# Optimization experiments

Measured on AMD Instinct MI355X. Metric: run time of the kernel, lower is better.

Reference implementation:

```python
import jax, jax.numpy as jnp
from jax import lax
import numpy as np

N_LAYERS = 4
D_MODEL = 512
EXPAND = 3
D_INNER = EXPAND * D_MODEL  # 1536
D_STATE = 32
D_CONV = 4
DT_RANK = (D_MODEL + 15) // 16  # 32 (mamba default ceil(d_model/16))
BATCH = 1024
N_FEAT = 68
N_RAIN = 4
N_NONRAIN = N_FEAT - N_RAIN  # 64


def setup_inputs() -> dict:
    key = jax.random.key(0)
    ks = iter(jax.random.split(key, 40))

    def w(shape, s=0.02):
        return jax.random.normal(next(ks), shape, dtype=jnp.float32) * s

    inp = {
        'x': jax.random.normal(next(ks), (BATCH, N_FEAT), dtype=jnp.float32),
        # mamba_input_proj: Linear(64 -> d_model)
        'w_in': w((D_MODEL, N_NONRAIN)), 'b_in': jnp.zeros((D_MODEL,), jnp.float32),
        # per-layer LayerNorms
        'ln_g': jnp.ones((N_LAYERS, D_MODEL), jnp.float32),
        'ln_b': jnp.zeros((N_LAYERS, D_MODEL), jnp.float32),
        # Mamba per-layer params (stacked over layers)
        'W_inproj': w((N_LAYERS, 2 * D_INNER, D_MODEL)),
        'conv_w': w((N_LAYERS, D_INNER, D_CONV), 0.1),
        'conv_b': jnp.zeros((N_LAYERS, D_INNER), jnp.float32),
        'W_xproj': w((N_LAYERS, DT_RANK + 2 * D_STATE, D_INNER)),
        'W_dt': w((N_LAYERS, D_INNER, DT_RANK), 0.1),
        'b_dt': w((N_LAYERS, D_INNER), 0.5),
        'A_log': jnp.broadcast_to(jnp.log(jnp.arange(1, D_STATE + 1, dtype=jnp.float32)), (N_LAYERS, D_INNER, D_STATE)) + 0.0,
        'D_skip': jnp.ones((N_LAYERS, D_INNER), jnp.float32),
        'W_outproj': w((N_LAYERS, D_MODEL, D_INNER)),
        # logistic branch: Linear(4 -> 1) + sigmoid
        'w_log': w((1, N_RAIN), 0.1), 'b_log': jnp.zeros((1,), jnp.float32),
        # gate_proj: Linear(1 -> d_model)
        'W_gate': w((D_MODEL, 1), 0.1), 'b_gate': jnp.zeros((D_MODEL,), jnp.float32),
        # output head: Linear(d_model->32), ReLU, Linear(32->1)
        'W_h1': w((32, D_MODEL)), 'b_h1': jnp.zeros((32,), jnp.float32),
        'W_h2': w((1, 32)), 'b_h2': jnp.zeros((1,), jnp.float32),
    }
    return inp


def _layernorm(x, g, b, eps=1e-5):
    mu = x.mean(-1, keepdims=True)
    var = x.var(-1, keepdims=True)
    return (x - mu) * lax.rsqrt(var + eps) * g + b


def _mamba(x, Win, cw, cb, Wx, Wdt, bdt, Alog, Dp, Wout):
    # x: [B, L, d_model]
    B_, L, _ = x.shape
    xz = jnp.einsum('bld,ed->ble', x, Win)           # [B,L,2*d_inner]
    xc, z = jnp.split(xz, 2, axis=-1)
    # causal depthwise conv1d over L
    xt = jnp.pad(xc.transpose(0, 2, 1), ((0, 0), (0, 0), (D_CONV - 1, 0)))
    conv = lax.conv_general_dilated(xt, cw[:, None, :], (1,), 'VALID',
                                    dimension_numbers=('NCH', 'OIH', 'NCH'),
                                    feature_group_count=D_INNER)
    u = jax.nn.silu((conv + cb[None, :, None]).transpose(0, 2, 1))  # [B,L,d_inner]
    x_dbl = jnp.einsum('bld,ed->ble', u, Wx)         # [B,L,dt_rank+2*d_state]
    dt = x_dbl[..., :DT_RANK]
    Bm = x_dbl[..., DT_RANK:DT_RANK + D_STATE]
    Cm = x_dbl[..., DT_RANK + D_STATE:]
    delta = jax.nn.softplus(jnp.einsum('blr,dr->bld', dt, Wdt) + bdt)  # [B,L,d_inner]
    A = -jnp.exp(Alog)                               # [d_inner, d_state]
    dA = jnp.exp(jnp.einsum('bld,dn->bldn', delta, A))
    dBu = jnp.einsum('bld,bln->bldn', delta * u, Bm)

    def step(h, inp):
        dA_t, dBu_t, C_t = inp
        h = dA_t * h + dBu_t                         # [B,d_inner,d_state]
        return h, jnp.einsum('bdn,bn->bd', h, C_t)

    h0 = jnp.zeros((B_, D_INNER, D_STATE), x.dtype)
    _, ys = lax.scan(step, h0, (dA.transpose(1, 0, 2, 3), dBu.transpose(1, 0, 2, 3), Cm.transpose(1, 0, 2)))
    y = ys.transpose(1, 0, 2) + u * Dp               # [B,L,d_inner]
    y = y * jax.nn.silu(z)
    return jnp.einsum('bld,ed->ble', y, Wout)        # [B,L,d_model]


def reference(x, w_in, b_in, ln_g, ln_b, W_inproj, conv_w, conv_b, W_xproj, W_dt, b_dt,
              A_log, D_skip, W_outproj, w_log, b_log, W_gate, b_gate, W_h1, b_h1, W_h2, b_h2):
    rain = x[:, :N_RAIN]
    nonrain = x[:, N_RAIN:]
    h = jax.nn.relu(nonrain @ w_in.T + b_in)[:, None, :]   # [B,1,d_model]
    for l in range(N_LAYERS):
        res = h
        hn = _layernorm(h, ln_g[l], ln_b[l])
        hn = _mamba(hn, W_inproj[l], conv_w[l], conv_b[l], W_xproj[l], W_dt[l], b_dt[l],
                    A_log[l], D_skip[l], W_outproj[l])
        h = res + hn  # dropout is identity in eval mode
    m = h[:, 0, :]
    lg = jax.nn.sigmoid(rain @ w_log.T + b_log)            # [B,1]
    gate = lg @ W_gate.T + b_gate                          # [B,d_model]
    fused = m * gate
    z1 = jax.nn.relu(fused @ W_h1.T + b_h1)
    logits = (z1 @ W_h2.T + b_h2)[:, 0]
    return jax.nn.sigmoid(logits)
```

## Files before the change

### kernel.cpp

```cpp
#include <hip/hip_runtime.h>

typedef unsigned short u16;
typedef short v8s __attribute__((ext_vector_type(8)));
typedef float v4f __attribute__((ext_vector_type(4)));
typedef u16  v4u __attribute__((ext_vector_type(4)));

__device__ __forceinline__ float bf2f(u16 h){ return __uint_as_float(((unsigned)h)<<16); }
__device__ __forceinline__ u16 f2bf(float f){
  unsigned u = __float_as_uint(f);
  u += 0x7FFFu + ((u>>16)&1u);
  return (u16)(u>>16);
}
__device__ __forceinline__ float siluf(float x){ return x/(1.f+__expf(-x)); }
__device__ __forceinline__ float softplusf(float x){
  return (x>15.f) ? x : __logf(1.f+__expf(x));
}

struct SetupP {
  const float *x,*w_in,*b_in,*ln_g,*ln_b,*W_inproj,*W_xproj,*W_dt,*W_outproj;
  u16 *wIn,*wX,*wDt,*wOut;
  float *sg,*cb,*h;
  u16 *hb;
};

__global__ __launch_bounds__(256) void setup_kernel(SetupP sp)
{
  __shared__ u16 As[64*72], Bs[64*72];
  const int blk = blockIdx.x, t = threadIdx.x;
  if(blk < 9984){
    const int c0=6291456, c1=c0+589824, c2=c1+196608;
    int i4 = (blk*256 + t)*4;
    float4 v; u16* dst;
    if(i4 < c0){
      v = *(const float4*)(sp.W_inproj + i4);
      int k = i4 & 511, l = (i4>>9)/3072;
      const float* gg = sp.ln_g + l*512 + k;
      v.x*=gg[0]; v.y*=gg[1]; v.z*=gg[2]; v.w*=gg[3];
      dst = sp.wIn + i4;
    } else if(i4 < c1){ int o=i4-c0; v=*(const float4*)(sp.W_xproj+o);   dst=sp.wX+o; }
    else if(i4 < c2){   int o=i4-c1; v=*(const float4*)(sp.W_dt+o);      dst=sp.wDt+o; }
    else {              int o=i4-c2; v=*(const float4*)(sp.W_outproj+o); dst=sp.wOut+o; }
    v4u pk={ f2bf(v.x), f2bf(v.y), f2bf(v.z), f2bf(v.w) };
    *(v4u*)dst = pk;
    return;
  }
  if(blk < 13056){
    int wid=t>>6, lane=t&63;
    int ridx = (blk-9984)*4 + wid;
    int l = ridx/3072;
    const float* wr = sp.W_inproj + (size_t)ridx*512;
    const float* gg = sp.ln_g + l*512;
    const float* bb = sp.ln_b + l*512;
    float sgv=0.f, cbv=0.f;
#pragma unroll
    for(int i=0;i<8;i++){ int k=lane*8+i; float w=wr[k]; sgv+=gg[k]*w; cbv+=bb[k]*w; }
#pragma unroll
    for(int off=1; off<64; off<<=1){ sgv+=__shfl_xor(sgv,off); cbv+=__shfl_xor(cbv,off); }
    if(lane==0){ sp.sg[ridx]=sgv; sp.cb[ridx]=cbv; }
    return;
  }
  const int mb=blk-13056, mt=mb>>3, nt=mb&7;
  const int m0=mt*64, n0=nt*64;
  const int lane=t&63, wid=t>>6;
  const int wm=wid>>1, wn=wid&1, qd=lane>>4, lr=lane&15;
  const int r=t>>2, cq=t&3;
  {
    const float4* ax=(const float4*)(sp.x + (size_t)(m0+r)*68 + 4 + cq*16);
    const float4* bx=(const float4*)(sp.w_in + (size_t)(n0+r)*64 + cq*16);
    float4 av0=ax[0], av1=ax[1], av2=ax[2], av3=ax[3];
    float4 bv0=bx[0], bv1=bx[1], bv2=bx[2], bv3=bx[3];
    v4u pa0={f2bf(av0.x),f2bf(av0.y),f2bf(av0.z),f2bf(av0.w)};
    v4u pa1={f2bf(av1.x),f2bf(av1.y),f2bf(av1.z),f2bf(av1.w)};
    v4u pa2={f2bf(av2.x),f2bf(av2.y),f2bf(av2.z),f2bf(av2.w)};
    v4u pa3={f2bf(av3.x),f2bf(av3.y),f2bf(av3.z),f2bf(av3.w)};
    v4u pb0={f2bf(bv0.x),f2bf(bv0.y),f2bf(bv0.z),f2bf(bv0.w)};
    v4u pb1={f2bf(bv1.x),f2bf(bv1.y),f2bf(bv1.z),f2bf(bv1.w)};
    v4u pb2={f2bf(bv2.x),f2bf(bv2.y),f2bf(bv2.z),f2bf(bv2.w)};
    v4u pb3={f2bf(bv3.x),f2bf(bv3.y),f2bf(bv3.z),f2bf(bv3.w)};
    u16* aw=As+r*72+cq*16; u16* bw=Bs+r*72+cq*16;
    *(v4u*)(aw)=pa0; *(v4u*)(aw+4)=pa1; *(v4u*)(aw+8)=pa2; *(v4u*)(aw+12)=pa3;
    *(v4u*)(bw)=pb0; *(v4u*)(bw+4)=pb1; *(v4u*)(bw+8)=pb2; *(v4u*)(bw+12)=pb3;
  }
  __syncthreads();
  v4f acc[2][2];
#pragma unroll
  for(int i=0;i<2;i++)
#pragma unroll
    for(int j=0;j<2;j++) acc[i][j]=v4f{0.f,0.f,0.f,0.f};
#pragma unroll
  for(int s=0;s<2;s++){
    v8s af[2], bfv[2];
#pragma unroll
    for(int i=0;i<2;i++) af[i] =*(const v8s*)(As+(wm*32+i*16+lr)*72+s*32+qd*8);
#pragma unroll
    for(int j=0;j<2;j++) bfv[j]=*(const v8s*)(Bs+(wn*32+j*16+lr)*72+s*32+qd*8);
#pragma unroll
    for(int i=0;i<2;i++)
#pragma unroll
      for(int j=0;j<2;j++)
        acc[i][j]=__builtin_amdgcn_mfma_f32_16x16x32_bf16(af[i],bfv[j],acc[i][j],0,0,0);
  }
#pragma unroll
  for(int i=0;i<2;i++)
#pragma unroll
    for(int j=0;j<2;j++){
      const int gb0=m0+wm*32+i*16+qd*4;
      const int ge =n0+wn*32+j*16+lr;
#pragma unroll
      for(int rr=0;rr<4;rr++){
        float hv=fmaxf(acc[i][j][rr]+sp.b_in[ge],0.f);
        const size_t idx=(size_t)(gb0+rr)*512+ge;
        sp.h[idx]=hv; sp.hb[idx]=f2bf(hv);
      }
    }
}

__global__ __launch_bounds__(256) void gemm1_ln(
  const u16* __restrict__ hb, const u16* __restrict__ Wp,
  const float* __restrict__ sg, const float* __restrict__ cb,
  const float* __restrict__ convw, const float* __restrict__ convb,
  u16* __restrict__ u, u16* __restrict__ zs)
{
  __shared__ u16 As[64*72], Bs[64*72];
  __shared__ float sS1[64], sS2[64];
  const int tid=threadIdx.x, lane=tid&63, wid=tid>>6;
  const int wm=wid>>1, wn=wid&1, qd=lane>>4, lr=lane&15;
  const int m0=blockIdx.y*64, n0=blockIdx.x*64;
  const int r_=tid>>2, cq=tid&3;
  const u16* Ap = hb + (size_t)(m0+r_)*512 + cq*16;
  const u16* Bp = Wp + (size_t)(n0+r_)*512 + cq*16;
  u16* Asw = As + r_*72 + cq*16;
  u16* Bsw = Bs + r_*72 + cq*16;

  v4f acc[2][2];
#pragma unroll
  for(int i=0;i<2;i++)
#pragma unroll
    for(int j=0;j<2;j++) acc[i][j]=v4f{0.f,0.f,0.f,0.f};
  float s1=0.f, s2=0.f;

  auto statAcc=[&](v8s v){
#pragma unroll
    for(int e=0;e<8;e++){ float f=bf2f((u16)v[e]); s1+=f; s2+=f*f; }
  };
  auto domfma=[&](){
#pragma unroll
    for(int s=0;s<2;s++){
      v8s af[2], bfv[2];
#pragma unroll
      for(int i=0;i<2;i++) af[i] =*(const v8s*)(As+(wm*32+i*16+lr)*72+s*32+qd*8);
#pragma unroll
      for(int j=0;j<2;j++) bfv[j]=*(const v8s*)(Bs+(wn*32+j*16+lr)*72+s*32+qd*8);
#pragma unroll
      for(int i=0;i<2;i++)
#pragma unroll
        for(int j=0;j<2;j++)
          acc[i][j]=__builtin_amdgcn_mfma_f32_16x16x32_bf16(af[i],bfv[j],acc[i][j],0,0,0);
    }
  };

  v8s a0a=*(const v8s*)(Ap),    a0b=*(const v8s*)(Ap+8);
  v8s b0a=*(const v8s*)(Bp),    b0b=*(const v8s*)(Bp+8);
  v8s a1a=*(const v8s*)(Ap+64), a1b=*(const v8s*)(Ap+72);
  v8s b1a=*(const v8s*)(Bp+64), b1b=*(const v8s*)(Bp+72);
  for(int c=0;c<8;c+=2){
    __syncthreads();
    *(v8s*)Asw=a0a; *(v8s*)(Asw+8)=a0b;
    *(v8s*)Bsw=b0a; *(v8s*)(Bsw+8)=b0b;
    statAcc(a0a); statAcc(a0b);
    __syncthreads();
    if(c+2<8){
      a0a=*(const v8s*)(Ap+(c+2)*64); a0b=*(const v8s*)(Ap+(c+2)*64+8);
      b0a=*(const v8s*)(Bp+(c+2)*64); b0b=*(const v8s*)(Bp+(c+2)*64+8);
    }
    domfma();
    __syncthreads();
    *(v8s*)Asw=a1a; *(v8s*)(Asw+8)=a1b;
    *(v8s*)Bsw=b1a; *(v8s*)(Bsw+8)=b1b;
    statAcc(a1a); statAcc(a1b);
    __syncthreads();
    if(c+3<8){
      a1a=*(const v8s*)(Ap+(c+3)*64); a1b=*(const v8s*)(Ap+(c+3)*64+8);
      b1a=*(const v8s*)(Bp+(c+3)*64); b1b=*(const v8s*)(Bp+(c+3)*64+8);
    }
    domfma();
  }

  s1+=__shfl_xor(s1,1); s2+=__shfl_xor(s2,1);
  s1+=__shfl_xor(s1,2); s2+=__shfl_xor(s2,2);
  if(cq==0){ sS1[r_]=s1; sS2[r_]=s2; }
  __syncthreads();

#pragma unroll
  for(int i=0;i<2;i++){
    const int lb0=wm*32+i*16+qd*4;
#pragma unroll
    for(int r=0;r<4;r++){
      const int lb=lb0+r, gb=m0+lb;
      float mu=sS1[lb]*(1.f/512.f);
      float rs=rsqrtf(sS2[lb]*(1.f/512.f)-mu*mu+1e-5f);
#pragma unroll
      for(int j=0;j<2;j++){
        const int ge=n0+wn*32+j*16+lr;
        float val = rs*(acc[i][j][r] - mu*sg[ge]) + cb[ge];
        if(ge<1536){
          u[(size_t)gb*1536+ge]=f2bf(siluf(val*convw[ge*4+3]+convb[ge]));
        }else{
          zs[(size_t)gb*1536+(ge-1536)]=f2bf(siluf(val));
        }
      }
    }
  }
}

__global__ __launch_bounds__(256) void gemm2(
  const u16* __restrict__ A, const u16* __restrict__ wX,
  float* __restrict__ xpart)
{
  __shared__ u16 As[64*40];
  __shared__ u16 Bs[96*40];
  const int tid=threadIdx.x, lane=tid&63, wid=tid>>6;
  const int wm=wid>>1, wn=wid&1, qd=lane>>4, lr=lane&15;
  const int m0=blockIdx.y*64;
  const int k0=blockIdx.x*192;
  const int r_=tid>>2, kg_=tid&3;
  const u16* Ap  = A  + (size_t)(m0+r_)*1536 + k0 + kg_*8;
  const u16* Bp0 = wX + (size_t)r_*1536      + k0 + kg_*8;
  const u16* Bp1 = wX + (size_t)(64+r_)*1536 + k0 + kg_*8;
  u16* Asw  = As + r_*40 + kg_*8;
  u16* Bsw0 = Bs + r_*40 + kg_*8;
  u16* Bsw1 = Bs + (64+r_)*40 + kg_*8;
  const bool hasB1 = tid<128;

  v4f acc[2][3];
#pragma unroll
  for(int i=0;i<2;i++)
#pragma unroll
    for(int j=0;j<3;j++) acc[i][j]=v4f{0.f,0.f,0.f,0.f};

  auto domfma=[&](){
    v8s af[2], bfv[3];
#pragma unroll
    for(int i=0;i<2;i++) af[i] =*(const v8s*)(As+(wm*32+i*16+lr)*40+qd*8);
#pragma unroll
    for(int j=0;j<3;j++) bfv[j]=*(const v8s*)(Bs+(wn*48+j*16+lr)*40+qd*8);
#pragma unroll
    for(int i=0;i<2;i++)
#pragma unroll
      for(int j=0;j<3;j++)
        acc[i][j]=__builtin_amdgcn_mfma_f32_16x16x32_bf16(af[i],bfv[j],acc[i][j],0,0,0);
  };

  v8s a0=*(const v8s*)(Ap),    b0x=*(const v8s*)(Bp0),    b0y{};
  v8s a1=*(const v8s*)(Ap+32), b1x=*(const v8s*)(Bp0+32), b1y{};
  if(hasB1){ b0y=*(const v8s*)(Bp1); b1y=*(const v8s*)(Bp1+32); }
  for(int it=0; it<6; it+=2){
    const int kk=it*32;
    __syncthreads();
    *(v8s*)Asw=a0; *(v8s*)Bsw0=b0x; if(hasB1) *(v8s*)Bsw1=b0y;
    __syncthreads();
    if(it+2<6){ a0=*(const v8s*)(Ap+kk+64); b0x=*(const v8s*)(Bp0+kk+64);
      if(hasB1) b0y=*(const v8s*)(Bp1+kk+64); }
    domfma();
    __syncthreads();
    *(v8s*)Asw=a1; *(v8s*)Bsw0=b1x; if(hasB1) *(v8s*)Bsw1=b1y;
    __syncthreads();
    if(it+2<6){ a1=*(const v8s*)(Ap+kk+96); b1x=*(const v8s*)(Bp0+kk+96);
      if(hasB1) b1y=*(const v8s*)(Bp1+kk+96); }
    domfma();
  }

  float* op = xpart + (size_t)blockIdx.x*98304;
#pragma unroll
  for(int i=0;i<2;i++)
#pragma unroll
    for(int j=0;j<3;j++){
      const int gb0=m0+wm*32+i*16+qd*4;
      const int ge =wn*48+j*16+lr;
#pragma unroll
      for(int r=0;r<4;r++)
        op[(size_t)(gb0+r)*96+ge]=acc[i][j][r];
    }
}

__global__ __launch_bounds__(256) void gemm3(
  const float* __restrict__ xpart, const u16* __restrict__ wDt,
  const float* __restrict__ bdt, const float* __restrict__ Dp,
  const u16* __restrict__ u, const u16* __restrict__ zs,
  u16* __restrict__ y)
{
  __shared__ u16 dts[64*40];
  __shared__ u16 Bs[64*40];
  __shared__ float sbl[64];
  const int tid=threadIdx.x, lane=tid&63, wid=tid>>6;
  const int wm=wid>>1, wn=wid&1, qd=lane>>4, lr=lane&15;
  const int m0=blockIdx.y*64, n0=blockIdx.x*64;
  const int r=tid>>2, sub=tid&3;

  v8s breg = *(const v8s*)(wDt + (size_t)(n0+r)*32 + sub*8);

  float a24[24];
#pragma unroll
  for(int i=0;i<24;i++) a24[i]=0.f;
#pragma unroll
  for(int z=0;z<8;z++){
    const float4* bz=(const float4*)(xpart + (size_t)z*98304 + (size_t)(m0+r)*96);
#pragma unroll
    for(int t=0;t<6;t++){
      float4 v=bz[sub+4*t];
      a24[4*t]+=v.x; a24[4*t+1]+=v.y; a24[4*t+2]+=v.z; a24[4*t+3]+=v.w;
    }
  }
  float s_=0.f;
#pragma unroll
  for(int m=0;m<4;m++) s_ += a24[8+m]*a24[16+m] + a24[12+m]*a24[20+m];
  s_ += __shfl_xor(s_,1); s_ += __shfl_xor(s_,2);
  if(sub==0) sbl[r]=s_;
  v4u p0={ f2bf(a24[0]), f2bf(a24[1]), f2bf(a24[2]), f2bf(a24[3]) };
  v4u p1={ f2bf(a24[4]), f2bf(a24[5]), f2bf(a24[6]), f2bf(a24[7]) };
  *(v4u*)(dts + r*40 + 4*sub)      = p0;
  *(v4u*)(dts + r*40 + 16 + 4*sub) = p1;
  *(v8s*)(Bs + r*40 + sub*8) = breg;
  __syncthreads();

  v4f acc[2][2];
#pragma unroll
  for(int i=0;i<2;i++)
#pragma unroll
    for(int j=0;j<2;j++) acc[i][j]=v4f{0.f,0.f,0.f,0.f};
  v8s af[2], bfv[2];
#pragma unroll
  for(int i=0;i<2;i++) af[i] =*(const v8s*)(dts+(wm*32+i*16+lr)*40+qd*8);
#pragma unroll
  for(int j=0;j<2;j++) bfv[j]=*(const v8s*)(Bs+(wn*32+j*16+lr)*40+qd*8);
#pragma unroll
  for(int i=0;i<2;i++)
#pragma unroll
    for(int j=0;j<2;j++)
      acc[i][j]=__builtin_amdgcn_mfma_f32_16x16x32_bf16(af[i],bfv[j],acc[i][j],0,0,0);

#pragma unroll
  for(int i=0;i<2;i++){
    const int lb0=wm*32+i*16+qd*4;
#pragma unroll
    for(int rr=0;rr<4;rr++){
      const int gb=m0+lb0+rr;
      const float sv=sbl[lb0+rr];
#pragma unroll
      for(int j=0;j<2;j++){
        const int ge=n0+wn*32+j*16+lr;
        float delta=softplusf(acc[i][j][rr]+bdt[ge]);
        float uu=bf2f(u[(size_t)gb*1536+ge]);
        float zz=bf2f(zs[(size_t)gb*1536+ge]);
        y[(size_t)gb*1536+ge]=f2bf(uu*(delta*sv+Dp[ge])*zz);
      }
    }
  }
}

__global__ __launch_bounds__(256) void gemm4(
  const u16* __restrict__ yv, const u16* __restrict__ wO,
  float* __restrict__ h, u16* __restrict__ hb)
{
  __shared__ u16 As[32*72], Bs[32*72];
  const int tid=threadIdx.x, lane=tid&63, wid=tid>>6;
  const int wm=wid>>1, wn=wid&1, qd=lane>>4, lr=lane&15;
  const int m0=blockIdx.y*32, n0=blockIdx.x*32;
  const int half=tid>>7, ts=tid&127;
  const int r_=ts>>2, cq=ts&3;
  const u16* Gp = (half ? wO + (size_t)(n0+r_)*1536
                        : yv + (size_t)(m0+r_)*1536) + cq*16;
  u16* Sw = (half ? Bs : As) + r_*72 + cq*16;

  v4f acc=v4f{0.f,0.f,0.f,0.f};
  auto domfma=[&](){
#pragma unroll
    for(int s=0;s<2;s++){
      v8s af=*(const v8s*)(As+(wm*16+lr)*72+s*32+qd*8);
      v8s bf=*(const v8s*)(Bs+(wn*16+lr)*72+s*32+qd*8);
      acc=__builtin_amdgcn_mfma_f32_16x16x32_bf16(af,bf,acc,0,0,0);
    }
  };

  v8s g0a=*(const v8s*)(Gp),    g0b=*(const v8s*)(Gp+8);
  v8s g1a=*(const v8s*)(Gp+64), g1b=*(const v8s*)(Gp+72);
  for(int c=0;c<24;c+=2){
    __syncthreads();
    *(v8s*)Sw=g0a; *(v8s*)(Sw+8)=g0b;
    __syncthreads();
    if(c+2<24){ g0a=*(const v8s*)(Gp+(c+2)*64); g0b=*(const v8s*)(Gp+(c+2)*64+8); }
    domfma();
    __syncthreads();
    *(v8s*)Sw=g1a; *(v8s*)(Sw+8)=g1b;
    __syncthreads();
    if(c+3<24){ g1a=*(const v8s*)(Gp+(c+3)*64); g1b=*(const v8s*)(Gp+(c+3)*64+8); }
    domfma();
  }

#pragma unroll
  for(int r=0;r<4;r++){
    const int gb=m0+wm*16+qd*4+r;
    const int ge=n0+wn*16+lr;
    const size_t idx=(size_t)gb*512+ge;
    float hv=h[idx]+acc[r];
    h[idx]=hv; hb[idx]=f2bf(hv);
  }
}

__global__ __launch_bounds__(256) void head_kernel(
  const float* __restrict__ x, const float* __restrict__ h,
  const float* __restrict__ wlog, const float* __restrict__ blog,
  const float* __restrict__ wg, const float* __restrict__ bg,
  const float* __restrict__ wh1, const float* __restrict__ bh1,
  const float* __restrict__ wh2, const float* __restrict__ bh2,
  float* __restrict__ out)
{
  int b = blockIdx.x, t = threadIdx.x;
  __shared__ float fused[512];
  __shared__ float part[256];
  __shared__ float z1s[32];
  float lgin = x[b*68+0]*wlog[0] + x[b*68+1]*wlog[1]
             + x[b*68+2]*wlog[2] + x[b*68+3]*wlog[3] + blog[0];
  float lg = 1.f/(1.f+__expf(-lgin));
  for(int d=t; d<512; d+=256)
    fused[d] = h[(size_t)b*512+d]*(lg*wg[d] + bg[d]);
  __syncthreads();
  int j = t&31, c = t>>5;
  float p = 0.f;
#pragma unroll
  for(int i=0;i<64;i++){ int d = c*64+i; p += fused[d]*wh1[j*512+d]; }
  part[t] = p;
  __syncthreads();
  if(t < 32){
    float z = bh1[t];
#pragma unroll
    for(int cc=0; cc<8; cc++) z += part[cc*32+t];
    z1s[t] = fmaxf(z, 0.f);
  }
  __syncthreads();
  if(t==0){
    float lo = bh2[0];
#pragma unroll
    for(int jj=0;jj<32;jj++) lo += z1s[jj]*wh2[jj];
    out[b] = 1.f/(1.f+__expf(-lo));
  }
}

extern "C" void kernel_launch(void* const* d_in, const int* in_sizes, int n_in,
                              void* d_out, int out_size, void* d_ws, size_t ws_size,
                              hipStream_t stream)
{
  const float* x        = (const float*)d_in[0];
  const float* w_in     = (const float*)d_in[1];
  const float* b_in     = (const float*)d_in[2];
  const float* ln_g     = (const float*)d_in[3];
  const float* ln_b     = (const float*)d_in[4];
  const float* W_inproj = (const float*)d_in[5];
  const float* conv_w   = (const float*)d_in[6];
  const float* conv_b   = (const float*)d_in[7];
  const float* W_xproj  = (const float*)d_in[8];
  const float* W_dt     = (const float*)d_in[9];
  const float* b_dt     = (const float*)d_in[10];
  const float* D_skip   = (const float*)d_in[12];
  const float* W_outproj= (const float*)d_in[13];
  const float* w_log    = (const float*)d_in[14];
  const float* b_log    = (const float*)d_in[15];
  const float* W_gate   = (const float*)d_in[16];
  const float* b_gate   = (const float*)d_in[17];
  const float* W_h1     = (const float*)d_in[18];
  const float* b_h1     = (const float*)d_in[19];
  const float* W_h2     = (const float*)d_in[20];
  const float* b_h2     = (const float*)d_in[21];
  float* out = (float*)d_out;
  (void)in_sizes; (void)n_in; (void)out_size; (void)ws_size;

  char* ws = (char*)d_ws;
  size_t off = 0;
  auto alloc = [&](size_t bytes)->char*{
    char* p = ws + off; off = (off + bytes + 255) & ~(size_t)255; return p; };
  u16*   wIn  = (u16*)  alloc(6291456u*2);
  u16*   wX   = (u16*)  alloc(589824u*2);
  u16*   wDt  = (u16*)  alloc(196608u*2);
  u16*   wOut = (u16*)  alloc(3145728u*2);
  float* sg   = (float*)alloc(12288u*4);
  float* cb   = (float*)alloc(12288u*4);
  float* h    = (float*)alloc(524288u*4);
  u16*   hb   = (u16*)  alloc(524288u*2);
  u16*   u    = (u16*)  alloc(1572864u*2);
  u16*   zs   = (u16*)  alloc(1572864u*2);
  u16*   y    = (u16*)  alloc(1572864u*2);
  float* xpart= (float*)alloc(8u*98304u*4);

  SetupP sp;
  sp.x=x; sp.w_in=w_in; sp.b_in=b_in; sp.ln_g=ln_g; sp.ln_b=ln_b;
  sp.W_inproj=W_inproj; sp.W_xproj=W_xproj; sp.W_dt=W_dt; sp.W_outproj=W_outproj;
  sp.wIn=wIn; sp.wX=wX; sp.wDt=wDt; sp.wOut=wOut;
  sp.sg=sg; sp.cb=cb; sp.h=h; sp.hb=hb;

  setup_kernel<<<13184,256,0,stream>>>(sp);

  for(int l=0;l<4;l++){
    gemm1_ln<<<dim3(48,16),256,0,stream>>>(
      hb, wIn+(size_t)l*1572864, sg+l*3072, cb+l*3072,
      conv_w+l*6144, conv_b+l*1536, u, zs);
    gemm2<<<dim3(8,16),256,0,stream>>>(
      u, wX+(size_t)l*147456, xpart);
    gemm3<<<dim3(24,16),256,0,stream>>>(
      xpart, wDt+(size_t)l*49152, b_dt+l*1536, D_skip+l*1536, u, zs, y);
    gemm4<<<dim3(16,32),256,0,stream>>>(
      y, wOut+(size_t)l*786432, h, hb);
  }

  head_kernel<<<1024,256,0,stream>>>(x, h, w_log, b_log, W_gate, b_gate,
                                     W_h1, b_h1, W_h2, b_h2, out);
}
```

Before: 288.4 us.

## Enlarge gemm1 M tile to 128 rows and double gemm4 K step

The input-projection GEMM with fused LayerNorm now covers 128 batch rows per block instead of 64, so each wave computes a 64x32 output from more accumulators and each weight tile loaded is reused across twice as many rows. The grid is halved in the y dimension to match. The output-projection GEMM now stages a K chunk of 128 per iteration instead of 64, which halves the number of barrier pairs and widens each load. In exchange, registers and shared memory per block go up and there are fewer blocks, which may reduce occupancy and leave some compute units idle.

```diff
diff --git a/kernel.cpp b/kernel.cpp
--- a/kernel.cpp
+++ b/kernel.cpp
@@ -121,20 +121,21 @@
   const float* __restrict__ convw, const float* __restrict__ convb,
   u16* __restrict__ u, u16* __restrict__ zs)
 {
-  __shared__ u16 As[64*72], Bs[64*72];
-  __shared__ float sS1[64], sS2[64];
+  __shared__ u16 As[128*72], Bs[64*72];
+  __shared__ float sS1[128], sS2[128];
   const int tid=threadIdx.x, lane=tid&63, wid=tid>>6;
   const int wm=wid>>1, wn=wid&1, qd=lane>>4, lr=lane&15;
-  const int m0=blockIdx.y*64, n0=blockIdx.x*64;
-  const int r_=tid>>2, cq=tid&3;
-  const u16* Ap = hb + (size_t)(m0+r_)*512 + cq*16;
-  const u16* Bp = Wp + (size_t)(n0+r_)*512 + cq*16;
-  u16* Asw = As + r_*72 + cq*16;
-  u16* Bsw = Bs + r_*72 + cq*16;
-
-  v4f acc[2][2];
-#pragma unroll
-  for(int i=0;i<2;i++)
+  const int m0=blockIdx.y*128, n0=blockIdx.x*64;
+  const int rA=tid>>1, cqA=tid&1;
+  const u16* Ap = hb + (size_t)(m0+rA)*512 + cqA*32;
+  u16* Asw = As + rA*72 + cqA*32;
+  const int rB=tid>>2, cqB=tid&3;
+  const u16* Bp = Wp + (size_t)(n0+rB)*512 + cqB*16;
+  u16* Bsw = Bs + rB*72 + cqB*16;
+
+  v4f acc[4][2];
+#pragma unroll
+  for(int i=0;i<4;i++)
 #pragma unroll
     for(int j=0;j<2;j++) acc[i][j]=v4f{0.f,0.f,0.f,0.f};
   float s1=0.f, s2=0.f;
@@ -146,54 +147,65 @@
   auto domfma=[&](){
 #pragma unroll
     for(int s=0;s<2;s++){
-      v8s af[2], bfv[2];
-#pragma unroll
-      for(int i=0;i<2;i++) af[i] =*(const v8s*)(As+(wm*32+i*16+lr)*72+s*32+qd*8);
+      v8s af[4], bfv[2];
+#pragma unroll
+      for(int i=0;i<4;i++) af[i] =*(const v8s*)(As+(wm*64+i*16+lr)*72+s*32+qd*8);
 #pragma unroll
       for(int j=0;j<2;j++) bfv[j]=*(const v8s*)(Bs+(wn*32+j*16+lr)*72+s*32+qd*8);
 #pragma unroll
-      for(int i=0;i<2;i++)
+      for(int i=0;i<4;i++)
 #pragma unroll
         for(int j=0;j<2;j++)
           acc[i][j]=__builtin_amdgcn_mfma_f32_16x16x32_bf16(af[i],bfv[j],acc[i][j],0,0,0);
     }
   };
 
-  v8s a0a=*(const v8s*)(Ap),    a0b=*(const v8s*)(Ap+8);
-  v8s b0a=*(const v8s*)(Bp),    b0b=*(const v8s*)(Bp+8);
-  v8s a1a=*(const v8s*)(Ap+64), a1b=*(const v8s*)(Ap+72);
-  v8s b1a=*(const v8s*)(Bp+64), b1b=*(const v8s*)(Bp+72);
+  v8s a0[4], a1[4], b0[2], b1[2];
+#pragma unroll
+  for(int q=0;q<4;q++){ a0[q]=*(const v8s*)(Ap+q*8); a1[q]=*(const v8s*)(Ap+64+q*8); }
+#pragma unroll
+  for(int q=0;q<2;q++){ b0[q]=*(const v8s*)(Bp+q*8); b1[q]=*(const v8s*)(Bp+64+q*8); }
+
   for(int c=0;c<8;c+=2){
     __syncthreads();
-    *(v8s*)Asw=a0a; *(v8s*)(Asw+8)=a0b;
-    *(v8s*)Bsw=b0a; *(v8s*)(Bsw+8)=b0b;
-    statAcc(a0a); statAcc(a0b);
+#pragma unroll
+    for(int q=0;q<4;q++) *(v8s*)(Asw+q*8)=a0[q];
+#pragma unroll
+    for(int q=0;q<2;q++) *(v8s*)(Bsw+q*8)=b0[q];
+#pragma unroll
+    for(int q=0;q<4;q++) statAcc(a0[q]);
     __syncthreads();
     if(c+2<8){
-      a0a=*(const v8s*)(Ap+(c+2)*64); a0b=*(const v8s*)(Ap+(c+2)*64+8);
-      b0a=*(const v8s*)(Bp+(c+2)*64); b0b=*(const v8s*)(Bp+(c+2)*64+8);
+#pragma unroll
+      for(int q=0;q<4;q++) a0[q]=*(const v8s*)(Ap+(c+2)*64+q*8);
+#pragma unroll
+      for(int q=0;q<2;q++) b0[q]=*(const v8s*)(Bp+(c+2)*64+q*8);
     }
     domfma();
     __syncthreads();
-    *(v8s*)Asw=a1a; *(v8s*)(Asw+8)=a1b;
-    *(v8s*)Bsw=b1a; *(v8s*)(Bsw+8)=b1b;
-    statAcc(a1a); statAcc(a1b);
+#pragma unroll
+    for(int q=0;q<4;q++) *(v8s*)(Asw+q*8)=a1[q];
+#pragma unroll
+    for(int q=0;q<2;q++) *(v8s*)(Bsw+q*8)=b1[q];
+#pragma unroll
+    for(int q=0;q<4;q++) statAcc(a1[q]);
     __syncthreads();
     if(c+3<8){
-      a1a=*(const v8s*)(Ap+(c+3)*64); a1b=*(const v8s*)(Ap+(c+3)*64+8);
-      b1a=*(const v8s*)(Bp+(c+3)*64); b1b=*(const v8s*)(Bp+(c+3)*64+8);
+#pragma unroll
+      for(int q=0;q<4;q++) a1[q]=*(const v8s*)(Ap+(c+3)*64+q*8);
+#pragma unroll
+      for(int q=0;q<2;q++) b1[q]=*(const v8s*)(Bp+(c+3)*64+q*8);
     }
     domfma();
   }
 
   s1+=__shfl_xor(s1,1); s2+=__shfl_xor(s2,1);
-  s1+=__shfl_xor(s1,2); s2+=__shfl_xor(s2,2);
-  if(cq==0){ sS1[r_]=s1; sS2[r_]=s2; }
+  if(cqA==0){ sS1[rA]=s1; sS2[rA]=s2; }
   __syncthreads();
 
 #pragma unroll
-  for(int i=0;i<2;i++){
-    const int lb0=wm*32+i*16+qd*4;
+  for(int i=0;i<4;i++){
+    const int lb0=wm*64+i*16+qd*4;
 #pragma unroll
     for(int r=0;r<4;r++){
       const int lb=lb0+r, gb=m0+lb;
@@ -362,38 +374,47 @@
   const u16* __restrict__ yv, const u16* __restrict__ wO,
   float* __restrict__ h, u16* __restrict__ hb)
 {
-  __shared__ u16 As[32*72], Bs[32*72];
+  __shared__ u16 As[32*136], Bs[32*136];
   const int tid=threadIdx.x, lane=tid&63, wid=tid>>6;
   const int wm=wid>>1, wn=wid&1, qd=lane>>4, lr=lane&15;
   const int m0=blockIdx.y*32, n0=blockIdx.x*32;
   const int half=tid>>7, ts=tid&127;
   const int r_=ts>>2, cq=ts&3;
   const u16* Gp = (half ? wO + (size_t)(n0+r_)*1536
-                        : yv + (size_t)(m0+r_)*1536) + cq*16;
-  u16* Sw = (half ? Bs : As) + r_*72 + cq*16;
+                        : yv + (size_t)(m0+r_)*1536) + cq*32;
+  u16* Sw = (half ? Bs : As) + r_*136 + cq*32;
 
   v4f acc=v4f{0.f,0.f,0.f,0.f};
   auto domfma=[&](){
 #pragma unroll
-    for(int s=0;s<2;s++){
-      v8s af=*(const v8s*)(As+(wm*16+lr)*72+s*32+qd*8);
-      v8s bf=*(const v8s*)(Bs+(wn*16+lr)*72+s*32+qd*8);
+    for(int s=0;s<4;s++){
+      v8s af=*(const v8s*)(As+(wm*16+lr)*136+s*32+qd*8);
+      v8s bf=*(const v8s*)(Bs+(wn*16+lr)*136+s*32+qd*8);
       acc=__builtin_amdgcn_mfma_f32_16x16x32_bf16(af,bf,acc,0,0,0);
     }
   };
 
-  v8s g0a=*(const v8s*)(Gp),    g0b=*(const v8s*)(Gp+8);
-  v8s g1a=*(const v8s*)(Gp+64), g1b=*(const v8s*)(Gp+72);
-  for(int c=0;c<24;c+=2){
-    __syncthreads();
-    *(v8s*)Sw=g0a; *(v8s*)(Sw+8)=g0b;
-    __syncthreads();
-    if(c+2<24){ g0a=*(const v8s*)(Gp+(c+2)*64); g0b=*(const v8s*)(Gp+(c+2)*64+8); }
+  v8s g0[4], g1[4];
+#pragma unroll
+  for(int q=0;q<4;q++){ g0[q]=*(const v8s*)(Gp+q*8); g1[q]=*(const v8s*)(Gp+128+q*8); }
+  for(int c=0;c<12;c+=2){
+    __syncthreads();
+#pragma unroll
+    for(int q=0;q<4;q++) *(v8s*)(Sw+q*8)=g0[q];
+    __syncthreads();
+    if(c+2<12){
+#pragma unroll
+      for(int q=0;q<4;q++) g0[q]=*(const v8s*)(Gp+(c+2)*128+q*8);
+    }
     domfma();
     __syncthreads();
-    *(v8s*)Sw=g1a; *(v8s*)(Sw+8)=g1b;
-    __syncthreads();
-    if(c+3<24){ g1a=*(const v8s*)(Gp+(c+3)*64); g1b=*(const v8s*)(Gp+(c+3)*64+8); }
+#pragma unroll
+    for(int q=0;q<4;q++) *(v8s*)(Sw+q*8)=g1[q];
+    __syncthreads();
+    if(c+3<12){
+#pragma unroll
+      for(int q=0;q<4;q++) g1[q]=*(const v8s*)(Gp+(c+3)*128+q*8);
+    }
     domfma();
   }
 
@@ -500,7 +521,7 @@
   setup_kernel<<<13184,256,0,stream>>>(sp);
 
   for(int l=0;l<4;l++){
-    gemm1_ln<<<dim3(48,16),256,0,stream>>>(
+    gemm1_ln<<<dim3(48,8),256,0,stream>>>(
       hb, wIn+(size_t)l*1572864, sg+l*3072, cb+l*3072,
       conv_w+l*6144, conv_b+l*1536, u, zs);
     gemm2<<<dim3(8,16),256,0,stream>>>(
```

After: 314.6 us. 9.1% more time.

## Use direct global-to-LDS loads with XOR swizzle and move LayerNorm stats upstream

Applied to the files above, without the earlier changes.

gemm1_ln and gemm4 now stage tiles with global_load_lds straight into XOR-swizzled shared memory instead of going through registers with padded rows. The register double-buffering is dropped, so each k-chunk loads and then computes in sequence. LayerNorm row sums and sums of squares are no longer computed inside gemm1_ln. They are accumulated by atomics in the epilogues of the producing kernels (setup_kernel and gemm4) into a stats buffer that is zeroed once per call. The aim is to cut VGPR staging and the per-element stat work in the GEMM main loop. The cost is atomics and shuffles in the epilogues, plus fp32 sums whose order now varies with atomic arrival.

```diff
diff --git a/kernel.cpp b/kernel.cpp
--- a/kernel.cpp
+++ b/kernel.cpp
@@ -15,11 +15,16 @@
 __device__ __forceinline__ float softplusf(float x){
   return (x>15.f) ? x : __logf(1.f+__expf(x));
 }
+__device__ __forceinline__ void gl16(const u16* g, u16* l){
+  __builtin_amdgcn_global_load_lds(
+    (const __attribute__((address_space(1))) void*)g,
+    (__attribute__((address_space(3))) void*)l, 16, 0, 0);
+}
 
 struct SetupP {
   const float *x,*w_in,*b_in,*ln_g,*ln_b,*W_inproj,*W_xproj,*W_dt,*W_outproj;
   u16 *wIn,*wX,*wDt,*wOut;
-  float *sg,*cb,*h;
+  float *sg,*cb,*h,*st0;
   u16 *hb;
 };
 
@@ -103,102 +108,82 @@
 #pragma unroll
   for(int i=0;i<2;i++)
 #pragma unroll
-    for(int j=0;j<2;j++){
-      const int gb0=m0+wm*32+i*16+qd*4;
-      const int ge =n0+wn*32+j*16+lr;
-#pragma unroll
-      for(int rr=0;rr<4;rr++){
-        float hv=fmaxf(acc[i][j][rr]+sp.b_in[ge],0.f);
-        const size_t idx=(size_t)(gb0+rr)*512+ge;
-        sp.h[idx]=hv; sp.hb[idx]=f2bf(hv);
-      }
+    for(int rr=0;rr<4;rr++){
+      const int gb=m0+wm*32+i*16+qd*4+rr;
+      const int ge0=n0+wn*32+lr, ge1=ge0+16;
+      float hv0=fmaxf(acc[i][0][rr]+sp.b_in[ge0],0.f);
+      float hv1=fmaxf(acc[i][1][rr]+sp.b_in[ge1],0.f);
+      sp.h[(size_t)gb*512+ge0]=hv0; sp.hb[(size_t)gb*512+ge0]=f2bf(hv0);
+      sp.h[(size_t)gb*512+ge1]=hv1; sp.hb[(size_t)gb*512+ge1]=f2bf(hv1);
+      float p1=hv0+hv1, p2=hv0*hv0+hv1*hv1;
+      p1+=__shfl_xor(p1,1); p2+=__shfl_xor(p2,1);
+      p1+=__shfl_xor(p1,2); p2+=__shfl_xor(p2,2);
+      p1+=__shfl_xor(p1,4); p2+=__shfl_xor(p2,4);
+      p1+=__shfl_xor(p1,8); p2+=__shfl_xor(p2,8);
+      if(lr==0){ atomicAdd(sp.st0+gb*2,p1); atomicAdd(sp.st0+gb*2+1,p2); }
     }
 }
 
 __global__ __launch_bounds__(256) void gemm1_ln(
   const u16* __restrict__ hb, const u16* __restrict__ Wp,
   const float* __restrict__ sg, const float* __restrict__ cb,
+  const float* __restrict__ st,
   const float* __restrict__ convw, const float* __restrict__ convb,
   u16* __restrict__ u, u16* __restrict__ zs)
 {
-  __shared__ u16 As[64*72], Bs[64*72];
-  __shared__ float sS1[64], sS2[64];
+  __shared__ u16 As[64*64];
+  __shared__ u16 Bs[64*64];
   const int tid=threadIdx.x, lane=tid&63, wid=tid>>6;
   const int wm=wid>>1, wn=wid&1, qd=lane>>4, lr=lane&15;
   const int m0=blockIdx.y*64, n0=blockIdx.x*64;
-  const int r_=tid>>2, cq=tid&3;
-  const u16* Ap = hb + (size_t)(m0+r_)*512 + cq*16;
-  const u16* Bp = Wp + (size_t)(n0+r_)*512 + cq*16;
-  u16* Asw = As + r_*72 + cq*16;
-  u16* Bsw = Bs + r_*72 + cq*16;
+  const int s0=wid*128+lane, s1=s0+64;
+  const int r0=s0>>3, q0=(s0&7)^(r0&7);
+  const int r1=s1>>3, q1=(s1&7)^(r1&7);
+  const u16* gA0 = hb + (size_t)(m0+r0)*512 + q0*8;
+  const u16* gA1 = hb + (size_t)(m0+r1)*512 + q1*8;
+  const u16* gB0 = Wp + (size_t)(n0+r0)*512 + q0*8;
+  const u16* gB1 = Wp + (size_t)(n0+r1)*512 + q1*8;
+  const int wb = __builtin_amdgcn_readfirstlane(wid);
+  u16* lA0 = As + wb*1024;  u16* lA1 = As + wb*1024 + 512;
+  u16* lB0 = Bs + wb*1024;  u16* lB1 = Bs + wb*1024 + 512;
 
   v4f acc[2][2];
 #pragma unroll
   for(int i=0;i<2;i++)
 #pragma unroll
     for(int j=0;j<2;j++) acc[i][j]=v4f{0.f,0.f,0.f,0.f};
-  float s1=0.f, s2=0.f;
-
-  auto statAcc=[&](v8s v){
-#pragma unroll
-    for(int e=0;e<8;e++){ float f=bf2f((u16)v[e]); s1+=f; s2+=f*f; }
-  };
-  auto domfma=[&](){
+  const int pxb = lr&7;
+
+#pragma unroll
+  for(int c=0;c<8;c++){
+    __syncthreads();
+    gl16(gA0 + c*64, lA0); gl16(gA1 + c*64, lA1);
+    gl16(gB0 + c*64, lB0); gl16(gB1 + c*64, lB1);
+    __syncthreads();
 #pragma unroll
     for(int s=0;s<2;s++){
+      const int px=(s*4+qd)^pxb;
       v8s af[2], bfv[2];
 #pragma unroll
-      for(int i=0;i<2;i++) af[i] =*(const v8s*)(As+(wm*32+i*16+lr)*72+s*32+qd*8);
-#pragma unroll
-      for(int j=0;j<2;j++) bfv[j]=*(const v8s*)(Bs+(wn*32+j*16+lr)*72+s*32+qd*8);
+      for(int i=0;i<2;i++) af[i] =*(const v8s*)(As+(wm*32+i*16+lr)*64+px*8);
+#pragma unroll
+      for(int j=0;j<2;j++) bfv[j]=*(const v8s*)(Bs+(wn*32+j*16+lr)*64+px*8);
 #pragma unroll
       for(int i=0;i<2;i++)
 #pragma unroll
         for(int j=0;j<2;j++)
           acc[i][j]=__builtin_amdgcn_mfma_f32_16x16x32_bf16(af[i],bfv[j],acc[i][j],0,0,0);
     }
-  };
-
-  v8s a0a=*(const v8s*)(Ap),    a0b=*(const v8s*)(Ap+8);
-  v8s b0a=*(const v8s*)(Bp),    b0b=*(const v8s*)(Bp+8);
-  v8s a1a=*(const v8s*)(Ap+64), a1b=*(const v8s*)(Ap+72);
-  v8s b1a=*(const v8s*)(Bp+64), b1b=*(const v8s*)(Bp+72);
-  for(int c=0;c<8;c+=2){
-    __syncthreads();
-    *(v8s*)Asw=a0a; *(v8s*)(Asw+8)=a0b;
-    *(v8s*)Bsw=b0a; *(v8s*)(Bsw+8)=b0b;
-    statAcc(a0a); statAcc(a0b);
-    __syncthreads();
-    if(c+2<8){
-      a0a=*(const v8s*)(Ap+(c+2)*64); a0b=*(const v8s*)(Ap+(c+2)*64+8);
-      b0a=*(const v8s*)(Bp+(c+2)*64); b0b=*(const v8s*)(Bp+(c+2)*64+8);
-    }
-    domfma();
-    __syncthreads();
-    *(v8s*)Asw=a1a; *(v8s*)(Asw+8)=a1b;
-    *(v8s*)Bsw=b1a; *(v8s*)(Bsw+8)=b1b;
-    statAcc(a1a); statAcc(a1b);
-    __syncthreads();
-    if(c+3<8){
-      a1a=*(const v8s*)(Ap+(c+3)*64); a1b=*(const v8s*)(Ap+(c+3)*64+8);
-      b1a=*(const v8s*)(Bp+(c+3)*64); b1b=*(const v8s*)(Bp+(c+3)*64+8);
-    }
-    domfma();
-  }
-
-  s1+=__shfl_xor(s1,1); s2+=__shfl_xor(s2,1);
-  s1+=__shfl_xor(s1,2); s2+=__shfl_xor(s2,2);
-  if(cq==0){ sS1[r_]=s1; sS2[r_]=s2; }
-  __syncthreads();
+  }
 
 #pragma unroll
   for(int i=0;i<2;i++){
-    const int lb0=wm*32+i*16+qd*4;
+    const int gb0=m0+wm*32+i*16+qd*4;
 #pragma unroll
     for(int r=0;r<4;r++){
-      const int lb=lb0+r, gb=m0+lb;
-      float mu=sS1[lb]*(1.f/512.f);
-      float rs=rsqrtf(sS2[lb]*(1.f/512.f)-mu*mu+1e-5f);
+      const int gb=gb0+r;
+      float mu=st[gb*2]*(1.f/512.f);
+      float rs=rsqrtf(st[gb*2+1]*(1.f/512.f)-mu*mu+1e-5f);
 #pragma unroll
       for(int j=0;j<2;j++){
         const int ge=n0+wn*32+j*16+lr;
@@ -360,41 +345,35 @@
 
 __global__ __launch_bounds__(256) void gemm4(
   const u16* __restrict__ yv, const u16* __restrict__ wO,
-  float* __restrict__ h, u16* __restrict__ hb)
-{
-  __shared__ u16 As[32*72], Bs[32*72];
+  float* __restrict__ h, u16* __restrict__ hb, float* __restrict__ stn)
+{
+  __shared__ u16 As[32*64], Bs[32*64];
   const int tid=threadIdx.x, lane=tid&63, wid=tid>>6;
   const int wm=wid>>1, wn=wid&1, qd=lane>>4, lr=lane&15;
   const int m0=blockIdx.y*32, n0=blockIdx.x*32;
-  const int half=tid>>7, ts=tid&127;
-  const int r_=ts>>2, cq=ts&3;
-  const u16* Gp = (half ? wO + (size_t)(n0+r_)*1536
-                        : yv + (size_t)(m0+r_)*1536) + cq*16;
-  u16* Sw = (half ? Bs : As) + r_*72 + cq*16;
+  const int s0=wid*64+lane;
+  const int r0=s0>>3, q0=(s0&7)^(r0&7);
+  const u16* gA = yv + (size_t)(m0+r0)*1536 + q0*8;
+  const u16* gB = wO + (size_t)(n0+r0)*1536 + q0*8;
+  const int wb = __builtin_amdgcn_readfirstlane(wid);
+  u16* lA = As + wb*512;
+  u16* lB = Bs + wb*512;
 
   v4f acc=v4f{0.f,0.f,0.f,0.f};
-  auto domfma=[&](){
+  const int pxb=lr&7;
+
+#pragma unroll
+  for(int c=0;c<24;c++){
+    __syncthreads();
+    gl16(gA + c*64, lA); gl16(gB + c*64, lB);
+    __syncthreads();
 #pragma unroll
     for(int s=0;s<2;s++){
-      v8s af=*(const v8s*)(As+(wm*16+lr)*72+s*32+qd*8);
-      v8s bf=*(const v8s*)(Bs+(wn*16+lr)*72+s*32+qd*8);
+      const int px=(s*4+qd)^pxb;
+      v8s af=*(const v8s*)(As+(wm*16+lr)*64+px*8);
+      v8s bf=*(const v8s*)(Bs+(wn*16+lr)*64+px*8);
       acc=__builtin_amdgcn_mfma_f32_16x16x32_bf16(af,bf,acc,0,0,0);
     }
-  };
-
-  v8s g0a=*(const v8s*)(Gp),    g0b=*(const v8s*)(Gp+8);
-  v8s g1a=*(const v8s*)(Gp+64), g1b=*(const v8s*)(Gp+72);
-  for(int c=0;c<24;c+=2){
-    __syncthreads();
-    *(v8s*)Sw=g0a; *(v8s*)(Sw+8)=g0b;
-    __syncthreads();
-    if(c+2<24){ g0a=*(const v8s*)(Gp+(c+2)*64); g0b=*(const v8s*)(Gp+(c+2)*64+8); }
-    domfma();
-    __syncthreads();
-    *(v8s*)Sw=g1a; *(v8s*)(Sw+8)=g1b;
-    __syncthreads();
-    if(c+3<24){ g1a=*(const v8s*)(Gp+(c+3)*64); g1b=*(const v8s*)(Gp+(c+3)*64+8); }
-    domfma();
   }
 
 #pragma unroll
@@ -404,6 +383,12 @@
     const size_t idx=(size_t)gb*512+ge;
     float hv=h[idx]+acc[r];
     h[idx]=hv; hb[idx]=f2bf(hv);
+    float p1=hv, p2=hv*hv;
+    p1+=__shfl_xor(p1,1); p2+=__shfl_xor(p2,1);
+    p1+=__shfl_xor(p1,2); p2+=__shfl_xor(p2,2);
+    p1+=__shfl_xor(p1,4); p2+=__shfl_xor(p2,4);
+    p1+=__shfl_xor(p1,8); p2+=__shfl_xor(p2,8);
+    if(lr==0){ atomicAdd(stn+gb*2,p1); atomicAdd(stn+gb*2+1,p2); }
   }
 }
 
@@ -484,6 +469,7 @@
   u16*   wOut = (u16*)  alloc(3145728u*2);
   float* sg   = (float*)alloc(12288u*4);
   float* cb   = (float*)alloc(12288u*4);
+  float* stats= (float*)alloc(10240u*4);
   float* h    = (float*)alloc(524288u*4);
   u16*   hb   = (u16*)  alloc(524288u*2);
   u16*   u    = (u16*)  alloc(1572864u*2);
@@ -491,24 +477,26 @@
   u16*   y    = (u16*)  alloc(1572864u*2);
   float* xpart= (float*)alloc(8u*98304u*4);
 
+  hipMemsetAsync(stats, 0, 10240u*4, stream);
+
   SetupP sp;
   sp.x=x; sp.w_in=w_in; sp.b_in=b_in; sp.ln_g=ln_g; sp.ln_b=ln_b;
   sp.W_inproj=W_inproj; sp.W_xproj=W_xproj; sp.W_dt=W_dt; sp.W_outproj=W_outproj;
   sp.wIn=wIn; sp.wX=wX; sp.wDt=wDt; sp.wOut=wOut;
-  sp.sg=sg; sp.cb=cb; sp.h=h; sp.hb=hb;
+  sp.sg=sg; sp.cb=cb; sp.h=h; sp.st0=stats; sp.hb=hb;
 
   setup_kernel<<<13184,256,0,stream>>>(sp);
 
   for(int l=0;l<4;l++){
     gemm1_ln<<<dim3(48,16),256,0,stream>>>(
-      hb, wIn+(size_t)l*1572864, sg+l*3072, cb+l*3072,
+      hb, wIn+(size_t)l*1572864, sg+l*3072, cb+l*3072, stats+l*2048,
       conv_w+l*6144, conv_b+l*1536, u, zs);
     gemm2<<<dim3(8,16),256,0,stream>>>(
       u, wX+(size_t)l*147456, xpart);
     gemm3<<<dim3(24,16),256,0,stream>>>(
       xpart, wDt+(size_t)l*49152, b_dt+l*1536, D_skip+l*1536, u, zs, y);
     gemm4<<<dim3(16,32),256,0,stream>>>(
-      y, wOut+(size_t)l*786432, h, hb);
+      y, wOut+(size_t)l*786432, h, hb, stats+(l+1)*2048);
   }
 
   head_kernel<<<1024,256,0,stream>>>(x, h, w_log, b_log, W_gate, b_gate,
```

After: 329.6 us. +14.3%, slower.
